# Optimization experiments

Measured on AMD Instinct MI355X. Metric: run time of the kernel, lower is better.

The kernel has to match this reference:

```python
import jax, jax.numpy as jnp
import numpy as np

N_NODES = 100000
N_EDGES = 1600000
IN_FEATS = 64
HIDDEN = 32
OUT_FEATS = 40


def _linear_init(key, fan_in, fan_out):
    kw, kb = jax.random.split(key)
    bound = 1.0 / np.sqrt(fan_in)
    W = jax.random.uniform(kw, (fan_in, fan_out), jnp.float32, -bound, bound)
    b = jax.random.uniform(kb, (fan_out,), jnp.float32, -bound, bound)
    return W, b


def setup_inputs() -> dict:
    key = jax.random.key(0)
    ks = jax.random.split(key, 8)
    x = jax.random.normal(ks[0], (N_NODES, IN_FEATS), jnp.float32)
    edge_index = jax.random.randint(ks[1], (2, N_EDGES), 0, N_NODES, jnp.int64)
    W_self1, b_self1 = _linear_init(ks[2], IN_FEATS, HIDDEN)
    W_neigh1, b_neigh1 = _linear_init(ks[3], IN_FEATS, HIDDEN)
    W_self2, b_self2 = _linear_init(ks[4], HIDDEN, HIDDEN)
    W_neigh2, b_neigh2 = _linear_init(ks[5], HIDDEN, HIDDEN)
    W_out, b_out = _linear_init(ks[6], HIDDEN, OUT_FEATS)
    W_lin1, b_lin1 = _linear_init(ks[7], IN_FEATS, OUT_FEATS)
    return {"x": x, "edge_index": edge_index,
            "W_self1": W_self1, "b_self1": b_self1,
            "W_neigh1": W_neigh1, "b_neigh1": b_neigh1,
            "W_self2": W_self2, "b_self2": b_self2,
            "W_neigh2": W_neigh2, "b_neigh2": b_neigh2,
            "W_out": W_out, "b_out": b_out,
            "W_lin1": W_lin1, "b_lin1": b_lin1}


def _scatter_mean(feats, src, dst, num_nodes):
    # gather neighbor features [E, F], sum into destinations, divide by degree
    msgs = feats[src]
    agg = jax.ops.segment_sum(msgs, dst, num_segments=num_nodes)
    cnt = jax.ops.segment_sum(jnp.ones((src.shape[0],), feats.dtype), dst,
                              num_segments=num_nodes)
    return agg / jnp.maximum(cnt, 1.0)[:, None]


def _intra_conv(h, src, dst, W_self, b_self, W_neigh, b_neigh, num_nodes):
    # scatter-mean aggregation + fused linear/residual(self)/relu
    x_self = h @ W_self + b_self
    neigh = _scatter_mean(h, src, dst, num_nodes)
    out = neigh @ W_neigh + b_neigh + x_self
    return jax.nn.relu(out)


def reference(x, edge_index, W_self1, b_self1, W_neigh1, b_neigh1,
              W_self2, b_self2, W_neigh2, b_neigh2, W_out, b_out,
              W_lin1, b_lin1):
    num_nodes = x.shape[0]
    src, dst = edge_index[0], edge_index[1]  # PyG source_to_target flow
    initial_x = x @ W_lin1 + b_lin1  # computed in original forward (unused in output)
    h = _intra_conv(x, src, dst, W_self1, b_self1, W_neigh1, b_neigh1, num_nodes)
    h = _intra_conv(h, src, dst, W_self2, b_self2, W_neigh2, b_neigh2, num_nodes)
    # hidden dim == 32 so x32 is the last layer's output (== h); dropout is eval no-op
    x32 = h
    logits = h @ W_out + b_out
    return (x32, logits)
```

## Files before the change

kernel.cpp:

```cpp
#include <hip/hip_runtime.h>

#define NN 100000
#define NE 1600000
#define RB 256
#define NPB 391
#define CAP 8192

typedef unsigned int uint;
typedef unsigned short ushort;
typedef __fp16 fp16x2 __attribute__((ext_vector_type(2)));

__device__ __forceinline__ float blo(uint u){ return __uint_as_float(u << 16); }
__device__ __forceinline__ float bhi(uint u){ return __uint_as_float(u & 0xffff0000u); }
__device__ __forceinline__ float b2f(ushort u){ return __uint_as_float(((uint)u) << 16); }
__device__ __forceinline__ ushort f2b(float f){
  uint u = __float_as_uint(f);
  uint r = (u + 0x7fffu + ((u >> 16) & 1u)) >> 16;
  return (ushort)r;
}
__device__ __forceinline__ uint packh2(float a, float b){
  union { fp16x2 h; uint u; } c; c.h = __builtin_amdgcn_cvt_pkrtz(a, b); return c.u;
}
__device__ __forceinline__ float h2lo(uint u){
  union { uint u; fp16x2 h; } c; c.u = u; return (float)c.h.x;
}
__device__ __forceinline__ float h2hi(uint u){
  union { uint u; fp16x2 h; } c; c.u = u; return (float)c.h.y;
}
__device__ __forceinline__ float ldf(const void* p, int i, bool isb){
  return isb ? b2f(((const ushort*)p)[i]) : ((const float*)p)[i];
}

__global__ void prep_k(const uint* __restrict__ xw,  const int* __restrict__ ei,
                       const void* __restrict__ Ws1, const void* __restrict__ bs1,
                       const void* __restrict__ Wn1, const void* __restrict__ bn1,
                       const void* __restrict__ Ws2, const void* __restrict__ bs2,
                       const void* __restrict__ Wn2, const void* __restrict__ bn2,
                       const void* __restrict__ Wo,  const void* __restrict__ bo,
                       float* __restrict__ wc1, float* __restrict__ bc1,
                       float* __restrict__ wc2, float* __restrict__ bc2,
                       float* __restrict__ wof, float* __restrict__ bof,
                       float* __restrict__ bn1f, float* __restrict__ bn2f,
                       int* __restrict__ flags, int* __restrict__ gcur)
{
  int t = threadIdx.x;
  __shared__ int nz, bcnt;
  __shared__ int s_isb, s_ei64;
  if (t == 0) { nz = 0; bcnt = 0; }
  __syncthreads();

  int hiw = ei[2 * t + 1];
  if (hiw != 0) atomicOr(&nz, 1);

  uint u = xw[t];
  uint le = (u >> 7) & 0xFFu;
  if (le == 0u || (le >= 96u && le <= 144u)) atomicAdd(&bcnt, 1);
  __syncthreads();
  if (t == 0) {
    s_ei64 = (nz == 0) ? 1 : 0;
    s_isb  = (bcnt >= 240) ? 1 : 0;
    flags[0] = s_isb;
    flags[1] = s_ei64;
  }
  __syncthreads();
  bool isb = (s_isb != 0);

  gcur[t] = t * CAP;

  for (int i = t; i < 64 * 64; i += 256) {
    int f = i >> 6, j = i & 63;
    wc1[i] = (j < 32) ? ldf(Ws1, f * 32 + j, isb) : ldf(Wn1, f * 32 + (j - 32), isb);
  }
  for (int i = t; i < 64; i += 256) bc1[i] = (i < 32) ? ldf(bs1, i, isb) : 0.f;
  for (int i = t; i < 32 * 64; i += 256) {
    int f = i >> 6, j = i & 63;
    wc2[i] = (j < 32) ? ldf(Ws2, f * 32 + j, isb) : ldf(Wn2, f * 32 + (j - 32), isb);
  }
  for (int i = t; i < 64; i += 256) bc2[i] = (i < 32) ? ldf(bs2, i, isb) : 0.f;
  for (int i = t; i < 32 * 40; i += 256) wof[i] = ldf(Wo, i, isb);
  for (int i = t; i < 40; i += 256) bof[i] = ldf(bo, i, isb);
  for (int i = t; i < 32; i += 256) bn1f[i] = ldf(bn1, i, isb);
  for (int i = t; i < 32; i += 256) bn2f[i] = ldf(bn2, i, isb);
}

__global__ __launch_bounds__(256) void part_k(const int* __restrict__ ei,
                                              const int* __restrict__ flags,
                                              int2* __restrict__ pairs,
                                              int* __restrict__ gcur, int E)
{
  __shared__ int hist[RB];
  __shared__ int gbase[RB];
  int m = flags[1];
  int base = blockIdx.x * 2048;
  hist[threadIdx.x] = 0;
  __syncthreads();
  int bk[8], rk[8]; int2 prs[8];
#pragma unroll
  for (int k = 0; k < 8; k++) {
    int e = base + threadIdx.x + k * 256;
    bk[k] = -1;
    if (e < E) {
      int d = m ? ei[2 * (E + e)] : ei[E + e];
      int s = m ? ei[2 * e] : ei[e];
      bk[k] = d / NPB;
      rk[k] = atomicAdd(&hist[bk[k]], 1);
      prs[k] = make_int2(d, s);
    }
  }
  __syncthreads();
  if (hist[threadIdx.x] > 0)
    gbase[threadIdx.x] = atomicAdd(&gcur[threadIdx.x], hist[threadIdx.x]);
  __syncthreads();
#pragma unroll
  for (int k = 0; k < 8; k++) {
    if (bk[k] >= 0) {
      int pos = gbase[bk[k]] + rk[k];
      if (pos < (bk[k] + 1) * CAP) pairs[pos] = prs[k];
    }
  }
}

__global__ __launch_bounds__(512) void csr_bucket_k(const int2* __restrict__ pairs,
                                                    const int* __restrict__ gcur,
                                                    int* __restrict__ rowptr,
                                                    int* __restrict__ col)
{
  __shared__ int lh[NPB];
  __shared__ int ps[512];
  __shared__ int cs[RB];
  int t = threadIdx.x;
  int r = blockIdx.x;
  if (t < RB) cs[t] = min(gcur[t] - t * CAP, CAP);
  __syncthreads();
  if (t < RB) ps[t] = cs[t];
  __syncthreads();
  for (int off = 1; off < RB; off <<= 1) {
    int v = (t < RB && t >= off) ? ps[t - off] : 0;
    __syncthreads();
    if (t < RB) ps[t] += v;
    __syncthreads();
  }
  int n    = cs[r];
  int base = ps[r] - n;
  if (r == 0 && t == 0) rowptr[NN] = NE;
  __syncthreads();

  int lo = r * NPB;
  int nn = min(NPB, NN - lo);
  int b0 = r * CAP;
  for (int j = t; j < NPB; j += 512) lh[j] = 0;
  __syncthreads();
  for (int i = b0 + t; i < b0 + n; i += 512)
    atomicAdd(&lh[pairs[i].x - lo], 1);
  __syncthreads();
  int v = (t < nn) ? lh[t] : 0;
  ps[t] = v;
  __syncthreads();
  for (int off = 1; off < 512; off <<= 1) {
    int x = (t >= off) ? ps[t - off] : 0;
    __syncthreads();
    ps[t] += x;
    __syncthreads();
  }
  int excl = base + ps[t] - v;
  if (t < nn) rowptr[lo + t] = excl;
  __syncthreads();
  if (t < nn) lh[t] = excl;
  __syncthreads();
  for (int i = b0 + t; i < b0 + n; i += 512) {
    int2 pr = pairs[i];
    int p = atomicAdd(&lh[pr.x - lo], 1);
    col[p] = pr.y;
  }
}

template <int IN, bool XDYN>
__global__ __launch_bounds__(256) void transform_split_k(const void* __restrict__ xin,
                                                         const float* __restrict__ W,
                                                         const float* __restrict__ bias,
                                                         float* __restrict__ tself,
                                                         uint* __restrict__ tneigh,
                                                         const int* __restrict__ flags, int N)
{
  int n = blockIdx.x * 256 + threadIdx.x;
  if (n >= N) return;
  bool isb = XDYN ? (flags[0] != 0) : false;
  float xr[IN];
  if (XDYN && isb) {
    const uint4* p = (const uint4*)((const ushort*)xin + (size_t)n * IN);
#pragma unroll
    for (int k = 0; k < IN / 8; k++) {
      uint4 v = p[k];
      xr[8 * k + 0] = blo(v.x); xr[8 * k + 1] = bhi(v.x);
      xr[8 * k + 2] = blo(v.y); xr[8 * k + 3] = bhi(v.y);
      xr[8 * k + 4] = blo(v.z); xr[8 * k + 5] = bhi(v.z);
      xr[8 * k + 6] = blo(v.w); xr[8 * k + 7] = bhi(v.w);
    }
  } else {
    const float4* p = (const float4*)((const float*)xin + (size_t)n * IN);
#pragma unroll
    for (int k = 0; k < IN / 4; k++) {
      float4 v = p[k];
      xr[4 * k + 0] = v.x; xr[4 * k + 1] = v.y; xr[4 * k + 2] = v.z; xr[4 * k + 3] = v.w;
    }
  }
#pragma unroll 1
  for (int j0 = 0; j0 < 64; j0 += 32) {
    float acc[32];
#pragma unroll
    for (int jj = 0; jj < 32; jj++) acc[jj] = bias[j0 + jj];
#pragma unroll 8
    for (int f = 0; f < IN; f++) {
      float xv = xr[f];
#pragma unroll
      for (int jj = 0; jj < 32; jj++)
        acc[jj] = fmaf(xv, W[f * 64 + j0 + jj], acc[jj]);
    }
    if (j0 == 0) {
      float* o = tself + (size_t)n * 32;
#pragma unroll
      for (int q = 0; q < 8; q++)
        ((float4*)o)[q] = make_float4(acc[4 * q], acc[4 * q + 1], acc[4 * q + 2], acc[4 * q + 3]);
    } else {
      uint* o = tneigh + (size_t)n * 16;
#pragma unroll
      for (int q = 0; q < 4; q++) {
        uint4 v;
        v.x = packh2(acc[8 * q + 0], acc[8 * q + 1]);
        v.y = packh2(acc[8 * q + 2], acc[8 * q + 3]);
        v.z = packh2(acc[8 * q + 4], acc[8 * q + 5]);
        v.w = packh2(acc[8 * q + 6], acc[8 * q + 7]);
        ((uint4*)o)[q] = v;
      }
    }
  }
}

__global__ __launch_bounds__(256) void aggregate_k(const float* __restrict__ tself,
                                                   const uint* __restrict__ tneigh,
                                                   const int* __restrict__ rowptr,
                                                   const int* __restrict__ col,
                                                   const float* __restrict__ bneigh,
                                                   float* __restrict__ hout,
                                                   void* __restrict__ out2,
                                                   const float* __restrict__ Wo,
                                                   const float* __restrict__ bo,
                                                   const int* __restrict__ flags, int N)
{
  __shared__ float hsh[4][32];
  int w = threadIdx.x >> 6;
  int d = blockIdx.x * 4 + w;
  int lane = threadIdx.x & 63;
  int slot = lane >> 4, f2 = lane & 15;
  int start = rowptr[d], end = rowptr[d + 1];
  int deg = end - start;
  float a0 = 0.f, a1 = 0.f;
  for (int base = start; base < end; base += 64) {
    int cnt = min(64, end - base);
    int ce = (lane < cnt) ? col[base + lane] : 0;
#pragma unroll 1
    for (int j = 0; j < cnt; j += 16) {
      int k0 = j + slot, k1 = j + 4 + slot, k2 = j + 8 + slot, k3 = j + 12 + slot;
      int i0 = __shfl(ce, k0, 64);
      int i1 = __shfl(ce, k1, 64);
      int i2 = __shfl(ce, k2, 64);
      int i3 = __shfl(ce, k3, 64);
      uint u0 = 0, u1 = 0, u2 = 0, u3 = 0;
      if (k0 < cnt) u0 = tneigh[(size_t)i0 * 16 + f2];
      if (k1 < cnt) u1 = tneigh[(size_t)i1 * 16 + f2];
      if (k2 < cnt) u2 = tneigh[(size_t)i2 * 16 + f2];
      if (k3 < cnt) u3 = tneigh[(size_t)i3 * 16 + f2];
      a0 += h2lo(u0) + h2lo(u1) + h2lo(u2) + h2lo(u3);
      a1 += h2hi(u0) + h2hi(u1) + h2hi(u2) + h2hi(u3);
    }
  }
  a0 += __shfl_down(a0, 32, 64); a1 += __shfl_down(a1, 32, 64);
  a0 += __shfl_down(a0, 16, 64); a1 += __shfl_down(a1, 16, 64);
  bool isb = (flags[0] != 0);
  if (lane < 16) {
    float scale = 1.0f / (float)max(deg, 1);
    float2 self = ((const float2*)(tself + (size_t)d * 32))[f2];
    float v0 = fmaxf(fmaf(a0, scale, bneigh[2 * f2]     + self.x), 0.f);
    float v1 = fmaxf(fmaf(a1, scale, bneigh[2 * f2 + 1] + self.y), 0.f);
    if (hout) ((float2*)(hout + (size_t)d * 32))[f2] = make_float2(v0, v1);
    if (out2) {
      if (isb) ((uint*)out2)[(size_t)d * 16 + f2] = (uint)f2b(v0) | ((uint)f2b(v1) << 16);
      else     ((float2*)out2)[(size_t)d * 16 + f2] = make_float2(v0, v1);
    }
    hsh[w][2 * f2] = v0; hsh[w][2 * f2 + 1] = v1;
  }
  if (Wo) {
    __syncthreads();
    if (lane < 40) {
      float acc = bo[lane];
#pragma unroll 8
      for (int f = 0; f < 32; f++)
        acc = fmaf(hsh[w][f], Wo[f * 40 + lane], acc);
      size_t idx = (size_t)N * 32 + (size_t)d * 40 + lane;
      if (isb) ((ushort*)out2)[idx] = f2b(acc);
      else     ((float*)out2)[idx] = acc;
    }
  }
}

extern "C" void kernel_launch(void* const* d_in, const int* in_sizes, int n_in,
                              void* d_out, int out_size, void* d_ws, size_t ws_size,
                              hipStream_t stream)
{
  const int N = NN, E = NE;
  const void* x   = d_in[0];
  const int*  ei  = (const int*)d_in[1];

  char* p = (char*)d_ws;
  auto alloc = [&](size_t bytes) -> void* {
    void* r = (void*)p;
    p += (bytes + 255) & ~(size_t)255;
    return r;
  };
  float* wc1  = (float*)alloc(64 * 64 * 4);
  float* bc1  = (float*)alloc(64 * 4);
  float* wc2  = (float*)alloc(32 * 64 * 4);
  float* bc2  = (float*)alloc(64 * 4);
  float* wof  = (float*)alloc(32 * 40 * 4);
  float* bof  = (float*)alloc(40 * 4);
  float* bn1f = (float*)alloc(32 * 4);
  float* bn2f = (float*)alloc(32 * 4);
  int*   flags = (int*)alloc(8);
  int*   gcur = (int*)alloc(RB * 4);
  int*   rowptr = (int*)alloc(((size_t)N + 1) * 4);
  int*   col  = (int*)alloc((size_t)E * 4);
  int2*  pairs = (int2*)alloc((size_t)RB * CAP * 8);
  float* tself  = (float*)alloc((size_t)N * 32 * 4);
  uint*  tneigh = (uint*)alloc((size_t)N * 16 * 4);
  float* hbuf = (float*)alloc((size_t)N * 32 * 4);

  prep_k<<<1, 256, 0, stream>>>((const uint*)x, ei,
                                d_in[2], d_in[3], d_in[4], d_in[5],
                                d_in[6], d_in[7], d_in[8], d_in[9],
                                d_in[10], d_in[11],
                                wc1, bc1, wc2, bc2, wof, bof, bn1f, bn2f,
                                flags, gcur);
  part_k<<<(E + 2047) / 2048, 256, 0, stream>>>(ei, flags, pairs, gcur, E);
  csr_bucket_k<<<RB, 512, 0, stream>>>(pairs, gcur, rowptr, col);

  transform_split_k<64, true><<<(N + 255) / 256, 256, 0, stream>>>(
      x, wc1, bc1, tself, tneigh, flags, N);
  aggregate_k<<<N / 4, 256, 0, stream>>>(tself, tneigh, rowptr, col, bn1f,
                                         hbuf, (void*)nullptr,
                                         (const float*)nullptr, (const float*)nullptr,
                                         flags, N);

  transform_split_k<32, false><<<(N + 255) / 256, 256, 0, stream>>>(
      hbuf, wc2, bc2, tself, tneigh, flags, N);
  aggregate_k<<<N / 4, 256, 0, stream>>>(tself, tneigh, rowptr, col, bn2f,
                                         (float*)nullptr, d_out,
                                         wof, bof, flags, N);
}
```

Measured before the change: 296.3 us.

## Widen aggregate gathers to 8-byte loads, store (start,deg) descriptors, parallelize prep

The aggregate kernel now assigns 8 lanes per neighbor row with uint2 loads (4 features per lane) instead of 16 lanes with 4-byte loads. That halves the gather instructions per edge, at the cost of fewer concurrent edges per wave. The CSR build writes an int2 (start, degree) descriptor per node in place of rowptr, so each node needs one load rather than two dependent ones. The weight-prep kernel now runs on 17 blocks with a grid-stride loop instead of a single block.

```diff
diff --git a/kernel.cpp b/kernel.cpp
--- a/kernel.cpp
+++ b/kernel.cpp
@@ -45,7 +45,7 @@
 {
   int t = threadIdx.x;
   __shared__ int nz, bcnt;
-  __shared__ int s_isb, s_ei64;
+  __shared__ int s_isb;
   if (t == 0) { nz = 0; bcnt = 0; }
   __syncthreads();
 
@@ -56,31 +56,31 @@
   uint le = (u >> 7) & 0xFFu;
   if (le == 0u || (le >= 96u && le <= 144u)) atomicAdd(&bcnt, 1);
   __syncthreads();
-  if (t == 0) {
-    s_ei64 = (nz == 0) ? 1 : 0;
-    s_isb  = (bcnt >= 240) ? 1 : 0;
-    flags[0] = s_isb;
-    flags[1] = s_ei64;
+  if (t == 0) s_isb = (bcnt >= 240) ? 1 : 0;
+  if (blockIdx.x == 0 && t == 0) {
+    flags[0] = (bcnt >= 240) ? 1 : 0;
+    flags[1] = (nz == 0) ? 1 : 0;
   }
   __syncthreads();
   bool isb = (s_isb != 0);
 
-  gcur[t] = t * CAP;
-
-  for (int i = t; i < 64 * 64; i += 256) {
+  if (blockIdx.x == 0) gcur[t] = t * CAP;
+
+  int g0 = blockIdx.x * 256 + t, gs = gridDim.x * 256;
+  for (int i = g0; i < 64 * 64; i += gs) {
     int f = i >> 6, j = i & 63;
     wc1[i] = (j < 32) ? ldf(Ws1, f * 32 + j, isb) : ldf(Wn1, f * 32 + (j - 32), isb);
   }
-  for (int i = t; i < 64; i += 256) bc1[i] = (i < 32) ? ldf(bs1, i, isb) : 0.f;
-  for (int i = t; i < 32 * 64; i += 256) {
+  for (int i = g0; i < 64; i += gs) bc1[i] = (i < 32) ? ldf(bs1, i, isb) : 0.f;
+  for (int i = g0; i < 32 * 64; i += gs) {
     int f = i >> 6, j = i & 63;
     wc2[i] = (j < 32) ? ldf(Ws2, f * 32 + j, isb) : ldf(Wn2, f * 32 + (j - 32), isb);
   }
-  for (int i = t; i < 64; i += 256) bc2[i] = (i < 32) ? ldf(bs2, i, isb) : 0.f;
-  for (int i = t; i < 32 * 40; i += 256) wof[i] = ldf(Wo, i, isb);
-  for (int i = t; i < 40; i += 256) bof[i] = ldf(bo, i, isb);
-  for (int i = t; i < 32; i += 256) bn1f[i] = ldf(bn1, i, isb);
-  for (int i = t; i < 32; i += 256) bn2f[i] = ldf(bn2, i, isb);
+  for (int i = g0; i < 64; i += gs) bc2[i] = (i < 32) ? ldf(bs2, i, isb) : 0.f;
+  for (int i = g0; i < 32 * 40; i += gs) wof[i] = ldf(Wo, i, isb);
+  for (int i = g0; i < 40; i += gs) bof[i] = ldf(bo, i, isb);
+  for (int i = g0; i < 32; i += gs) bn1f[i] = ldf(bn1, i, isb);
+  for (int i = g0; i < 32; i += gs) bn2f[i] = ldf(bn2, i, isb);
 }
 
 __global__ __launch_bounds__(256) void part_k(const int* __restrict__ ei,
@@ -122,7 +122,7 @@
 
 __global__ __launch_bounds__(512) void csr_bucket_k(const int2* __restrict__ pairs,
                                                     const int* __restrict__ gcur,
-                                                    int* __restrict__ rowptr,
+                                                    int2* __restrict__ desc,
                                                     int* __restrict__ col)
 {
   __shared__ int lh[NPB];
@@ -142,7 +142,6 @@
   }
   int n    = cs[r];
   int base = ps[r] - n;
-  if (r == 0 && t == 0) rowptr[NN] = NE;
   __syncthreads();
 
   int lo = r * NPB;
@@ -163,7 +162,7 @@
     __syncthreads();
   }
   int excl = base + ps[t] - v;
-  if (t < nn) rowptr[lo + t] = excl;
+  if (t < nn) desc[lo + t] = make_int2(excl, v);
   __syncthreads();
   if (t < nn) lh[t] = excl;
   __syncthreads();
@@ -238,7 +237,7 @@
 
 __global__ __launch_bounds__(256) void aggregate_k(const float* __restrict__ tself,
                                                    const uint* __restrict__ tneigh,
-                                                   const int* __restrict__ rowptr,
+                                                   const int2* __restrict__ desc,
                                                    const int* __restrict__ col,
                                                    const float* __restrict__ bneigh,
                                                    float* __restrict__ hout,
@@ -251,43 +250,55 @@
   int w = threadIdx.x >> 6;
   int d = blockIdx.x * 4 + w;
   int lane = threadIdx.x & 63;
-  int slot = lane >> 4, f2 = lane & 15;
-  int start = rowptr[d], end = rowptr[d + 1];
-  int deg = end - start;
-  float a0 = 0.f, a1 = 0.f;
+  int slot = lane >> 3, f4 = lane & 7;
+  int2 dd = desc[d];
+  int start = dd.x, deg = dd.y, end = start + deg;
+  float a0 = 0.f, a1 = 0.f, a2 = 0.f, a3 = 0.f;
   for (int base = start; base < end; base += 64) {
     int cnt = min(64, end - base);
     int ce = (lane < cnt) ? col[base + lane] : 0;
 #pragma unroll 1
     for (int j = 0; j < cnt; j += 16) {
-      int k0 = j + slot, k1 = j + 4 + slot, k2 = j + 8 + slot, k3 = j + 12 + slot;
+      int k0 = j + slot, k1 = j + 8 + slot;
       int i0 = __shfl(ce, k0, 64);
       int i1 = __shfl(ce, k1, 64);
-      int i2 = __shfl(ce, k2, 64);
-      int i3 = __shfl(ce, k3, 64);
-      uint u0 = 0, u1 = 0, u2 = 0, u3 = 0;
-      if (k0 < cnt) u0 = tneigh[(size_t)i0 * 16 + f2];
-      if (k1 < cnt) u1 = tneigh[(size_t)i1 * 16 + f2];
-      if (k2 < cnt) u2 = tneigh[(size_t)i2 * 16 + f2];
-      if (k3 < cnt) u3 = tneigh[(size_t)i3 * 16 + f2];
-      a0 += h2lo(u0) + h2lo(u1) + h2lo(u2) + h2lo(u3);
-      a1 += h2hi(u0) + h2hi(u1) + h2hi(u2) + h2hi(u3);
-    }
-  }
+      uint2 u0 = make_uint2(0, 0), u1 = make_uint2(0, 0);
+      if (k0 < cnt) u0 = ((const uint2*)(tneigh + (size_t)i0 * 16))[f4];
+      if (k1 < cnt) u1 = ((const uint2*)(tneigh + (size_t)i1 * 16))[f4];
+      a0 += h2lo(u0.x) + h2lo(u1.x);
+      a1 += h2hi(u0.x) + h2hi(u1.x);
+      a2 += h2lo(u0.y) + h2lo(u1.y);
+      a3 += h2hi(u0.y) + h2hi(u1.y);
+    }
+  }
+  a0 += __shfl_down(a0, 8, 64);  a1 += __shfl_down(a1, 8, 64);
+  a2 += __shfl_down(a2, 8, 64);  a3 += __shfl_down(a3, 8, 64);
+  a0 += __shfl_down(a0, 16, 64); a1 += __shfl_down(a1, 16, 64);
+  a2 += __shfl_down(a2, 16, 64); a3 += __shfl_down(a3, 16, 64);
   a0 += __shfl_down(a0, 32, 64); a1 += __shfl_down(a1, 32, 64);
-  a0 += __shfl_down(a0, 16, 64); a1 += __shfl_down(a1, 16, 64);
+  a2 += __shfl_down(a2, 32, 64); a3 += __shfl_down(a3, 32, 64);
   bool isb = (flags[0] != 0);
-  if (lane < 16) {
+  if (lane < 8) {
     float scale = 1.0f / (float)max(deg, 1);
-    float2 self = ((const float2*)(tself + (size_t)d * 32))[f2];
-    float v0 = fmaxf(fmaf(a0, scale, bneigh[2 * f2]     + self.x), 0.f);
-    float v1 = fmaxf(fmaf(a1, scale, bneigh[2 * f2 + 1] + self.y), 0.f);
-    if (hout) ((float2*)(hout + (size_t)d * 32))[f2] = make_float2(v0, v1);
+    float4 self = ((const float4*)(tself + (size_t)d * 32))[lane];
+    float4 bn   = ((const float4*)bneigh)[lane];
+    float v0 = fmaxf(fmaf(a0, scale, bn.x + self.x), 0.f);
+    float v1 = fmaxf(fmaf(a1, scale, bn.y + self.y), 0.f);
+    float v2 = fmaxf(fmaf(a2, scale, bn.z + self.z), 0.f);
+    float v3 = fmaxf(fmaf(a3, scale, bn.w + self.w), 0.f);
+    if (hout) ((float4*)(hout + (size_t)d * 32))[lane] = make_float4(v0, v1, v2, v3);
     if (out2) {
-      if (isb) ((uint*)out2)[(size_t)d * 16 + f2] = (uint)f2b(v0) | ((uint)f2b(v1) << 16);
-      else     ((float2*)out2)[(size_t)d * 16 + f2] = make_float2(v0, v1);
-    }
-    hsh[w][2 * f2] = v0; hsh[w][2 * f2 + 1] = v1;
+      if (isb) {
+        uint2 pk;
+        pk.x = (uint)f2b(v0) | ((uint)f2b(v1) << 16);
+        pk.y = (uint)f2b(v2) | ((uint)f2b(v3) << 16);
+        ((uint2*)out2)[(size_t)d * 8 + lane] = pk;
+      } else {
+        ((float4*)out2)[(size_t)d * 8 + lane] = make_float4(v0, v1, v2, v3);
+      }
+    }
+    hsh[w][4 * lane] = v0; hsh[w][4 * lane + 1] = v1;
+    hsh[w][4 * lane + 2] = v2; hsh[w][4 * lane + 3] = v3;
   }
   if (Wo) {
     __syncthreads();
@@ -327,32 +338,32 @@
   float* bn2f = (float*)alloc(32 * 4);
   int*   flags = (int*)alloc(8);
   int*   gcur = (int*)alloc(RB * 4);
-  int*   rowptr = (int*)alloc(((size_t)N + 1) * 4);
+  int2*  desc = (int2*)alloc((size_t)N * 8);
   int*   col  = (int*)alloc((size_t)E * 4);
   int2*  pairs = (int2*)alloc((size_t)RB * CAP * 8);
   float* tself  = (float*)alloc((size_t)N * 32 * 4);
   uint*  tneigh = (uint*)alloc((size_t)N * 16 * 4);
   float* hbuf = (float*)alloc((size_t)N * 32 * 4);
 
-  prep_k<<<1, 256, 0, stream>>>((const uint*)x, ei,
-                                d_in[2], d_in[3], d_in[4], d_in[5],
-                                d_in[6], d_in[7], d_in[8], d_in[9],
-                                d_in[10], d_in[11],
-                                wc1, bc1, wc2, bc2, wof, bof, bn1f, bn2f,
-                                flags, gcur);
+  prep_k<<<17, 256, 0, stream>>>((const uint*)x, ei,
+                                 d_in[2], d_in[3], d_in[4], d_in[5],
+                                 d_in[6], d_in[7], d_in[8], d_in[9],
+                                 d_in[10], d_in[11],
+                                 wc1, bc1, wc2, bc2, wof, bof, bn1f, bn2f,
+                                 flags, gcur);
   part_k<<<(E + 2047) / 2048, 256, 0, stream>>>(ei, flags, pairs, gcur, E);
-  csr_bucket_k<<<RB, 512, 0, stream>>>(pairs, gcur, rowptr, col);
+  csr_bucket_k<<<RB, 512, 0, stream>>>(pairs, gcur, desc, col);
 
   transform_split_k<64, true><<<(N + 255) / 256, 256, 0, stream>>>(
       x, wc1, bc1, tself, tneigh, flags, N);
-  aggregate_k<<<N / 4, 256, 0, stream>>>(tself, tneigh, rowptr, col, bn1f,
+  aggregate_k<<<N / 4, 256, 0, stream>>>(tself, tneigh, desc, col, bn1f,
                                          hbuf, (void*)nullptr,
                                          (const float*)nullptr, (const float*)nullptr,
                                          flags, N);
 
   transform_split_k<32, false><<<(N + 255) / 256, 256, 0, stream>>>(
       hbuf, wc2, bc2, tself, tneigh, flags, N);
-  aggregate_k<<<N / 4, 256, 0, stream>>>(tself, tneigh, rowptr, col, bn2f,
+  aggregate_k<<<N / 4, 256, 0, stream>>>(tself, tneigh, desc, col, bn2f,
                                          (float*)nullptr, d_out,
                                          wof, bof, flags, N);
 }
```

After: 287.4 us. 3.0% less time.
